# Kernel optimization log

Hardware: AMD Instinct MI355X
Metric: run time of the kernel (lower is better)

The kernel has to match this reference:

```python
import jax, jax.numpy as jnp
import numpy as np

WS = 5       # window_size
SHIFT = 2    # shift_size
NH = 3       # num_heads (hardcoded in module)
EPS = 1e-5   # LayerNorm eps (torch default)

B, H, W, C = 4, 400, 400, 48


def _window_partition(x, ws):
    b, h, w, c = x.shape
    x = x.reshape(b, h // ws, ws, w // ws, ws, c).transpose(0, 1, 3, 2, 4, 5)
    return x.reshape(-1, ws * ws, c)  # [B*nH*nW, ws*ws, C]


def _window_reverse(x, ws, h, w):
    bn = x.shape[0] // ((h // ws) * (w // ws))
    x = x.reshape(bn, h // ws, w // ws, ws, ws, -1).transpose(0, 1, 3, 2, 4, 5)
    return x.reshape(bn, h, w, -1)


def _qkv_branch(win, qkv_w, qkv_b, ln_g, ln_b):
    # Linear -> LayerNorm(last dim) -> Softmax over window-position axis (dim 1)
    y = win @ qkv_w + qkv_b                      # [B_, N, 3C]
    mu = jnp.mean(y, axis=-1, keepdims=True)
    var = jnp.mean((y - mu) ** 2, axis=-1, keepdims=True)
    y = (y - mu) * jax.lax.rsqrt(var + EPS) * ln_g + ln_b
    y = jax.nn.softmax(y, axis=1)                # nn.Softmax(1)
    b_, n, _ = y.shape
    y = y.reshape(b_, n, 3, NH, C // NH).transpose(2, 0, 3, 1, 4)  # [3, B_, h, N, d]
    return y[0], y[1], y[2]


def setup_inputs() -> dict:
    key = jax.random.key(0)
    ks = jax.random.split(key, 4)
    lr_patch = jax.random.normal(ks[0], (B, H, W, C), jnp.float32)
    ref_patch = jax.random.normal(ks[1], (B, H, W, C), jnp.float32)
    qkv_w = jax.random.normal(ks[2], (C, 3 * C), jnp.float32) * (1.0 / np.sqrt(C))
    qkv_b = jax.random.normal(ks[3], (3 * C,), jnp.float32) * 0.01
    ln_g = jnp.ones((3 * C,), jnp.float32)
    ln_b = jnp.zeros((3 * C,), jnp.float32)
    return {"lr_patch": lr_patch, "ref_patch": ref_patch, "qkv_w": qkv_w,
            "qkv_b": qkv_b, "ln_g": ln_g, "ln_b": ln_b}


def reference(lr_patch, ref_patch, qkv_w, qkv_b, ln_g, ln_b):
    # cyclic shift
    s_lr = jnp.roll(lr_patch, shift=(-SHIFT, -SHIFT), axis=(1, 2))
    s_ref = jnp.roll(ref_patch, shift=(-SHIFT, -SHIFT), axis=(1, 2))

    lr_w = _window_partition(s_lr, WS)    # [B_, N=25, C]
    ref_w = _window_partition(s_ref, WS)

    q_lr, k_lr, v_lr = _qkv_branch(lr_w, qkv_w, qkv_b, ln_g, ln_b)
    q_ref, k_ref, v_ref = _qkv_branch(ref_w, qkv_w, qkv_b, ln_g, ln_b)

    # dual cross-attention (no scaling / no second softmax, as in source)
    attn1 = jnp.einsum('bhnd,bhmd->bhnm', q_lr, k_ref)   # [B_, h, N, N]
    attn2 = jnp.einsum('bhnd,bhmd->bhnm', q_ref, k_lr)
    x = jnp.einsum('bhnm,bhmd->bhnd', attn1, v_ref)
    x = jnp.einsum('bhnm,bhmd->bhnd', attn2, x)

    b_, _, n, _ = x.shape
    x = x.transpose(0, 2, 1, 3).reshape(b_, n, C)        # [B_, N, C]
    x = x.reshape(-1, WS, WS, C)

    x = _window_reverse(x, WS, H, W)
    x = jnp.roll(x, shift=(SHIFT, SHIFT), axis=(1, 2))
    return (x, ref_patch)
```

## Files before the change

kernel.cpp:

```cpp
#include <hip/hip_runtime.h>
#include <hip/hip_bf16.h>

typedef __hip_bfloat16 hbf16;
typedef unsigned short ushort_t;
typedef __attribute__((ext_vector_type(8))) short bf16x8;
typedef __attribute__((ext_vector_type(4))) float f32x4;

#define WSZ 5
#define NWIN 25
#define CC 48
#define C3 144
#define HD 16
#define HDIM 400
#define NWH 80
#define SH 2
#define WPB 8
#define YW 152
#define WTW 56
#define PW 40

__device__ __forceinline__ ushort_t f2b(float x) {
    union { hbf16 h; ushort_t u; } c;
    c.h = __float2bfloat16(x);
    return c.u;
}
__device__ __forceinline__ float b2f_u(unsigned u) {
    union { unsigned i; float f; } c;
    c.i = u << 16;
    return c.f;
}
__device__ __forceinline__ unsigned pk2(float lo, float hi) {
    return ((unsigned)f2b(hi) << 16) | f2b(lo);
}

__global__ __launch_bounds__(256, 3) void swin_mfma(
    const float* __restrict__ lr, const float* __restrict__ ref,
    const float* __restrict__ qkv_w, const float* __restrict__ qkv_b,
    const float* __restrict__ ln_g, const float* __restrict__ ln_b,
    float* __restrict__ out)
{
    __shared__ __align__(16) ushort_t s_wT[C3 * WTW];
    __shared__ __align__(16) ushort_t s_y[64 * YW];
    __shared__ __align__(16) ushort_t s_vT[3 * 16 * PW];
    __shared__ __align__(16) ushort_t s_x1T[3 * 16 * PW];
    __shared__ __align__(16) ushort_t s_P[3 * 32 * PW];
    __shared__ float s_gb[3 * C3];

    const int tid  = threadIdx.x;
    const int wave = tid >> 6;
    const int lane = tid & 63;
    const int lm   = lane & 15;
    const int g    = lane >> 4;

    for (int i = tid; i < CC * C3; i += 256) {
        int c = i / C3, j = i % C3;
        s_wT[j * WTW + c] = f2b(qkv_w[i]);
    }
    for (int i = tid; i < C3; i += 256) {
        s_gb[i]           = qkv_b[i];
        s_gb[C3 + i]      = ln_g[i];
        s_gb[2 * C3 + i]  = ln_b[i];
    }
    for (int i = tid; i < 3 * 16 * PW; i += 256) { s_vT[i] = 0; s_x1T[i] = 0; }
    for (int i = tid; i < 3 * 32 * PW; i += 256) { s_P[i] = 0; }
    __syncthreads();

    const bf16x8 z8 = {0, 0, 0, 0, 0, 0, 0, 0};
    const f32x4  z4 = {0.f, 0.f, 0.f, 0.f};

    for (int it = 0; it < WPB; ++it) {
        const int wid = blockIdx.x * WPB + it;
        const int b   = wid / (NWH * NWH);
        const int rr  = wid % (NWH * NWH);
        const int bh  = rr / NWH;
        const int bw  = rr % NWH;

        const int pr = 16 * wave + lm;
        const bool vrow = (pr < 25) || (pr >= 32 && pr < 57);
        bf16x8 xa = z8, xb = z8;
        int n_row = (pr < 25) ? pr : pr - 32;
        {
            int wi = n_row / WSZ, wj = n_row % WSZ;
            int hh = bh * WSZ + wi + SH; if (hh >= HDIM) hh -= HDIM;
            int ww = bw * WSZ + wj + SH; if (ww >= HDIM) ww -= HDIM;
            const float* src = (pr < 32) ? lr : ref;
            const float* prow = src + ((size_t)(b * HDIM + hh) * HDIM + ww) * CC;
            if (vrow) {
                const float4* p4 = reinterpret_cast<const float4*>(prow);
                float4 u = p4[2 * g], v = p4[2 * g + 1];
                xa[0]=f2b(u.x); xa[1]=f2b(u.y); xa[2]=f2b(u.z); xa[3]=f2b(u.w);
                xa[4]=f2b(v.x); xa[5]=f2b(v.y); xa[6]=f2b(v.z); xa[7]=f2b(v.w);
                if (g < 2) {
                    float4 u2 = p4[8 + 2 * g], v2 = p4[9 + 2 * g];
                    xb[0]=f2b(u2.x); xb[1]=f2b(u2.y); xb[2]=f2b(u2.z); xb[3]=f2b(u2.w);
                    xb[4]=f2b(v2.x); xb[5]=f2b(v2.y); xb[6]=f2b(v2.z); xb[7]=f2b(v2.w);
                }
            }
        }

        f32x4 acc[9];
        const int ko2 = 32 + 8 * (g & 1);
        #pragma unroll
        for (int t = 0; t < 9; ++t) {
            const int col = 16 * t + lm;
            float bias = s_gb[col];
            f32x4 a = {bias, bias, bias, bias};
            bf16x8 w1 = *reinterpret_cast<const bf16x8*>(&s_wT[col * WTW + 8 * g]);
            a = __builtin_amdgcn_mfma_f32_16x16x32_bf16(xa, w1, a, 0, 0, 0);
            bf16x8 w2 = *reinterpret_cast<const bf16x8*>(&s_wT[col * WTW + ko2]);
            a = __builtin_amdgcn_mfma_f32_16x16x32_bf16(xb, w2, a, 0, 0, 0);
            acc[t] = a;
        }

        float mu[4], rs[4];
        #pragma unroll
        for (int r2 = 0; r2 < 4; ++r2) {
            float s = 0.f, sq = 0.f;
            #pragma unroll
            for (int t = 0; t < 9; ++t) { float v = acc[t][r2]; s += v; sq += v * v; }
            #pragma unroll
            for (int off = 8; off >= 1; off >>= 1) {
                s  += __shfl_xor(s, off);
                sq += __shfl_xor(sq, off);
            }
            float m = s * (1.f / 144.f);
            mu[r2] = m;
            rs[r2] = rsqrtf(sq * (1.f / 144.f) - m * m + 1e-5f);
        }

        const int prb = 16 * wave + 4 * g;
        #pragma unroll
        for (int t = 0; t < 9; ++t) {
            const int col = 16 * t + lm;
            const float gg = s_gb[C3 + col], bb = s_gb[2 * C3 + col];
            #pragma unroll
            for (int r2 = 0; r2 < 4; ++r2) {
                const int prow2 = prb + r2;
                const bool ok = (prow2 < 25) || (prow2 >= 32 && prow2 < 57);
                float yv = (acc[t][r2] - mu[r2]) * rs[r2] * gg + bb;
                ushort_t hv = ok ? f2b(yv) : (ushort_t)0;
                s_y[prow2 * YW + col] = hv;
            }
        }
        __syncthreads();

        #pragma unroll
        for (int ii = 0; ii < 2; ++ii) {
            const int item = wave * 72 + ii * 64 + lane;
            if (ii == 0 || lane < 8) {
                const int br  = item / C3;
                const int col = item % C3;
                const int base = br ? 32 : 0;
                float v[25];
                float mx = -1e30f;
                #pragma unroll
                for (int j = 0; j < 25; ++j) {
                    v[j] = b2f_u((unsigned)s_y[(base + j) * YW + col]);
                    mx = fmaxf(mx, v[j]);
                }
                float sum = 0.f;
                #pragma unroll
                for (int j = 0; j < 25; ++j) { v[j] = __expf(v[j] - mx); sum += v[j]; }
                float inv = 1.f / sum;
                #pragma unroll
                for (int j = 0; j < 25; ++j)
                    s_y[(base + j) * YW + col] = f2b(v[j] * inv);
            }
        }
        __syncthreads();

        for (int i = tid; i < 25 * CC; i += 256) {
            int m = i / CC, c = i % CC;
            int h2 = c >> 4, dv = c & 15;
            s_vT[h2 * (16 * PW) + dv * PW + m] = s_y[(32 + m) * YW + 96 + c];
        }
        __syncthreads();

        if (wave < 3) {
            const int h = wave;
            const int ko = 8 * (g & 1);
            f32x4 p1[2][2];
            bf16x8 ka0, ka1, qb0, qb1;
            {
                bf16x8 t0 = *reinterpret_cast<const bf16x8*>(&s_y[(32 + lm) * YW + CC + 16 * h + ko]);
                bf16x8 t1 = *reinterpret_cast<const bf16x8*>(&s_y[(48 + lm) * YW + CC + 16 * h + ko]);
                ka0 = (g < 2) ? t0 : z8;  ka1 = (g < 2) ? t1 : z8;
                bf16x8 t2 = *reinterpret_cast<const bf16x8*>(&s_y[lm * YW + 16 * h + ko]);
                bf16x8 t3 = *reinterpret_cast<const bf16x8*>(&s_y[(16 + lm) * YW + 16 * h + ko]);
                qb0 = (g < 2) ? t2 : z8;  qb1 = (g < 2) ? t3 : z8;
            }
            p1[0][0] = __builtin_amdgcn_mfma_f32_16x16x32_bf16(ka0, qb0, z4, 0, 0, 0);
            p1[0][1] = __builtin_amdgcn_mfma_f32_16x16x32_bf16(ka0, qb1, z4, 0, 0, 0);
            p1[1][0] = __builtin_amdgcn_mfma_f32_16x16x32_bf16(ka1, qb0, z4, 0, 0, 0);
            p1[1][1] = __builtin_amdgcn_mfma_f32_16x16x32_bf16(ka1, qb1, z4, 0, 0, 0);
            #pragma unroll
            for (int mt = 0; mt < 2; ++mt)
                #pragma unroll
                for (int nt = 0; nt < 2; ++nt) {
                    uint2 wv;
                    wv.x = pk2(p1[mt][nt][0], p1[mt][nt][1]);
                    wv.y = pk2(p1[mt][nt][2], p1[mt][nt][3]);
                    *reinterpret_cast<uint2*>(&s_P[h * (32 * PW) + (16 * nt + lm) * PW + 16 * mt + 4 * g]) = wv;
                }
            f32x4 x1a[2];
            {
                bf16x8 va = *reinterpret_cast<const bf16x8*>(&s_vT[h * (16 * PW) + lm * PW + 8 * g]);
                bf16x8 pb0 = *reinterpret_cast<const bf16x8*>(&s_P[h * (32 * PW) + lm * PW + 8 * g]);
                bf16x8 pb1 = *reinterpret_cast<const bf16x8*>(&s_P[h * (32 * PW) + (16 + lm) * PW + 8 * g]);
                x1a[0] = __builtin_amdgcn_mfma_f32_16x16x32_bf16(va, pb0, z4, 0, 0, 0);
                x1a[1] = __builtin_amdgcn_mfma_f32_16x16x32_bf16(va, pb1, z4, 0, 0, 0);
            }
            #pragma unroll
            for (int nt = 0; nt < 2; ++nt)
                #pragma unroll
                for (int r2 = 0; r2 < 4; ++r2)
                    s_x1T[h * (16 * PW) + (4 * g + r2) * PW + 16 * nt + lm] = f2b(x1a[nt][r2]);
            f32x4 p2[2][2];
            {
                bf16x8 t0 = *reinterpret_cast<const bf16x8*>(&s_y[lm * YW + CC + 16 * h + ko]);
                bf16x8 t1 = *reinterpret_cast<const bf16x8*>(&s_y[(16 + lm) * YW + CC + 16 * h + ko]);
                ka0 = (g < 2) ? t0 : z8;  ka1 = (g < 2) ? t1 : z8;
                bf16x8 t2 = *reinterpret_cast<const bf16x8*>(&s_y[(32 + lm) * YW + 16 * h + ko]);
                bf16x8 t3 = *reinterpret_cast<const bf16x8*>(&s_y[(48 + lm) * YW + 16 * h + ko]);
                qb0 = (g < 2) ? t2 : z8;  qb1 = (g < 2) ? t3 : z8;
            }
            p2[0][0] = __builtin_amdgcn_mfma_f32_16x16x32_bf16(ka0, qb0, z4, 0, 0, 0);
            p2[0][1] = __builtin_amdgcn_mfma_f32_16x16x32_bf16(ka0, qb1, z4, 0, 0, 0);
            p2[1][0] = __builtin_amdgcn_mfma_f32_16x16x32_bf16(ka1, qb0, z4, 0, 0, 0);
            p2[1][1] = __builtin_amdgcn_mfma_f32_16x16x32_bf16(ka1, qb1, z4, 0, 0, 0);
            #pragma unroll
            for (int mt = 0; mt < 2; ++mt)
                #pragma unroll
                for (int nt = 0; nt < 2; ++nt) {
                    uint2 wv;
                    wv.x = pk2(p2[mt][nt][0], p2[mt][nt][1]);
                    wv.y = pk2(p2[mt][nt][2], p2[mt][nt][3]);
                    *reinterpret_cast<uint2*>(&s_P[h * (32 * PW) + (16 * nt + lm) * PW + 16 * mt + 4 * g]) = wv;
                }
            {
                bf16x8 xv = *reinterpret_cast<const bf16x8*>(&s_x1T[h * (16 * PW) + lm * PW + 8 * g]);
                #pragma unroll
                for (int nt = 0; nt < 2; ++nt) {
                    bf16x8 pb = *reinterpret_cast<const bf16x8*>(&s_P[h * (32 * PW) + (16 * nt + lm) * PW + 8 * g]);
                    f32x4 x2a = __builtin_amdgcn_mfma_f32_16x16x32_bf16(xv, pb, z4, 0, 0, 0);
                    const int n = 16 * nt + lm;
                    if (n < 25) {
                        int wi = n / WSZ, wj = n % WSZ;
                        int oh = bh * WSZ + wi + SH; if (oh >= HDIM) oh -= HDIM;
                        int ow = bw * WSZ + wj + SH; if (ow >= HDIM) ow -= HDIM;
                        float4 o = make_float4(x2a[0], x2a[1], x2a[2], x2a[3]);
                        *reinterpret_cast<float4*>(
                            &out[((size_t)((b * HDIM + oh) * HDIM + ow)) * CC + 16 * h + 4 * g]) = o;
                    }
                }
            }
        }
        __syncthreads();
    }
}

__global__ void copy_ref_kernel(const float4* __restrict__ src, float4* __restrict__ dst,
                                long long n4) {
    long long i = (long long)blockIdx.x * blockDim.x + threadIdx.x;
    const long long stride = (long long)gridDim.x * blockDim.x;
    for (; i < n4; i += stride) dst[i] = src[i];
}

extern "C" void kernel_launch(void* const* d_in, const int* in_sizes, int n_in,
                              void* d_out, int out_size, void* d_ws, size_t ws_size,
                              hipStream_t stream) {
    const float* lr    = (const float*)d_in[0];
    const float* ref   = (const float*)d_in[1];
    const float* qkv_w = (const float*)d_in[2];
    const float* qkv_b = (const float*)d_in[3];
    const float* ln_g  = (const float*)d_in[4];
    const float* ln_b  = (const float*)d_in[5];
    float* out = (float*)d_out;

    const int n_blocks = 4 * NWH * NWH / WPB;
    swin_mfma<<<n_blocks, 256, 0, stream>>>(lr, ref, qkv_w, qkv_b, ln_g, ln_b, out);

    const size_t elems0 = (size_t)out_size / 2;
    const long long n4 = (long long)(elems0 / 4);
    copy_ref_kernel<<<2048, 256, 0, stream>>>(
        (const float4*)ref, (float4*)(out + elems0), n4);
}
```

Before: 329.7 us.

## Fuse ref passthrough copy into the main kernel and split QKV work across branch/column waves

```diff
diff --git a/kernel.cpp b/kernel.cpp
--- a/kernel.cpp
+++ b/kernel.cpp
@@ -2,15 +2,13 @@
 #include <hip/hip_bf16.h>
 
 typedef __hip_bfloat16 hbf16;
-typedef unsigned short ushort_t;
+typedef unsigned short u16t;
 typedef __attribute__((ext_vector_type(8))) short bf16x8;
 typedef __attribute__((ext_vector_type(4))) float f32x4;
 
 #define WSZ 5
-#define NWIN 25
 #define CC 48
 #define C3 144
-#define HD 16
 #define HDIM 400
 #define NWH 80
 #define SH 2
@@ -19,251 +17,239 @@
 #define WTW 56
 #define PW 40
 
-__device__ __forceinline__ ushort_t f2b(float x) {
-    union { hbf16 h; ushort_t u; } c;
+__device__ __forceinline__ u16t f2b(float x) {
+    union { hbf16 h; u16t u; } c;
     c.h = __float2bfloat16(x);
     return c.u;
 }
-__device__ __forceinline__ float b2f_u(unsigned u) {
-    union { unsigned i; float f; } c;
-    c.i = u << 16;
-    return c.f;
-}
 __device__ __forceinline__ unsigned pk2(float lo, float hi) {
     return ((unsigned)f2b(hi) << 16) | f2b(lo);
 }
 
-__global__ __launch_bounds__(256, 3) void swin_mfma(
+__global__ __launch_bounds__(256, 3) void swin_mfma2(
     const float* __restrict__ lr, const float* __restrict__ ref,
     const float* __restrict__ qkv_w, const float* __restrict__ qkv_b,
     const float* __restrict__ ln_g, const float* __restrict__ ln_b,
-    float* __restrict__ out)
+    float* __restrict__ out, float* __restrict__ out1)
 {
-    __shared__ __align__(16) ushort_t s_wT[C3 * WTW];
-    __shared__ __align__(16) ushort_t s_y[64 * YW];
-    __shared__ __align__(16) ushort_t s_vT[3 * 16 * PW];
-    __shared__ __align__(16) ushort_t s_x1T[3 * 16 * PW];
-    __shared__ __align__(16) ushort_t s_P[3 * 32 * PW];
-    __shared__ float s_gb[3 * C3];
-
-    const int tid  = threadIdx.x;
-    const int wave = tid >> 6;
-    const int lane = tid & 63;
-    const int lm   = lane & 15;
-    const int g    = lane >> 4;
+    __shared__ __align__(16) u16t s_wT[C3 * WTW];
+    __shared__ __align__(16) u16t s_y[64 * YW];
+    __shared__ __align__(16) u16t s_P[3 * 32 * PW];
+    __shared__ __align__(16) u16t s_x1T[3 * 16 * PW];
+    __shared__ __align__(16) float s_gb[3 * C3];
+    __shared__ __align__(16) float s_ln[4][16][4];
+
+    const int tid = threadIdx.x;
+    const int wave = tid >> 6, lane = tid & 63;
+    const int lm = lane & 15, g = lane >> 4;
+    const int br = wave >> 1, jh = wave & 1;
+    const int T0 = jh ? 4 : 0;
 
     for (int i = tid; i < CC * C3; i += 256) {
         int c = i / C3, j = i % C3;
         s_wT[j * WTW + c] = f2b(qkv_w[i]);
     }
     for (int i = tid; i < C3; i += 256) {
-        s_gb[i]           = qkv_b[i];
-        s_gb[C3 + i]      = ln_g[i];
-        s_gb[2 * C3 + i]  = ln_b[i];
+        s_gb[i] = qkv_b[i];
+        s_gb[C3 + i] = ln_g[i];
+        s_gb[2 * C3 + i] = ln_b[i];
     }
-    for (int i = tid; i < 3 * 16 * PW; i += 256) { s_vT[i] = 0; s_x1T[i] = 0; }
-    for (int i = tid; i < 3 * 32 * PW; i += 256) { s_P[i] = 0; }
     __syncthreads();
 
     const bf16x8 z8 = {0, 0, 0, 0, 0, 0, 0, 0};
     const f32x4  z4 = {0.f, 0.f, 0.f, 0.f};
+    const float* xsrc = br ? ref : lr;
 
     for (int it = 0; it < WPB; ++it) {
         const int wid = blockIdx.x * WPB + it;
-        const int b   = wid / (NWH * NWH);
-        const int rr  = wid % (NWH * NWH);
-        const int bh  = rr / NWH;
-        const int bw  = rr % NWH;
-
-        const int pr = 16 * wave + lm;
-        const bool vrow = (pr < 25) || (pr >= 32 && pr < 57);
-        bf16x8 xa = z8, xb = z8;
-        int n_row = (pr < 25) ? pr : pr - 32;
-        {
-            int wi = n_row / WSZ, wj = n_row % WSZ;
+        const int bb = wid / (NWH * NWH);
+        const int rr = wid % (NWH * NWH);
+        const int bh = rr / NWH, bw = rr % NWH;
+
+        bf16x8 xa[2], xb[2];
+        #pragma unroll
+        for (int s2 = 0; s2 < 2; ++s2) {
+            int row = 16 * s2 + lm;
+            int wi = row / WSZ, wj = row % WSZ;
             int hh = bh * WSZ + wi + SH; if (hh >= HDIM) hh -= HDIM;
             int ww = bw * WSZ + wj + SH; if (ww >= HDIM) ww -= HDIM;
-            const float* src = (pr < 32) ? lr : ref;
-            const float* prow = src + ((size_t)(b * HDIM + hh) * HDIM + ww) * CC;
-            if (vrow) {
-                const float4* p4 = reinterpret_cast<const float4*>(prow);
-                float4 u = p4[2 * g], v = p4[2 * g + 1];
-                xa[0]=f2b(u.x); xa[1]=f2b(u.y); xa[2]=f2b(u.z); xa[3]=f2b(u.w);
-                xa[4]=f2b(v.x); xa[5]=f2b(v.y); xa[6]=f2b(v.z); xa[7]=f2b(v.w);
-                if (g < 2) {
-                    float4 u2 = p4[8 + 2 * g], v2 = p4[9 + 2 * g];
-                    xb[0]=f2b(u2.x); xb[1]=f2b(u2.y); xb[2]=f2b(u2.z); xb[3]=f2b(u2.w);
-                    xb[4]=f2b(v2.x); xb[5]=f2b(v2.y); xb[6]=f2b(v2.z); xb[7]=f2b(v2.w);
+            const float4* p4 = reinterpret_cast<const float4*>(
+                xsrc + ((size_t)(bb * HDIM + hh) * HDIM + ww) * CC);
+            float4 u = p4[2 * g], v = p4[2 * g + 1];
+            bf16x8 t;
+            t[0] = f2b(u.x); t[1] = f2b(u.y); t[2] = f2b(u.z); t[3] = f2b(u.w);
+            t[4] = f2b(v.x); t[5] = f2b(v.y); t[6] = f2b(v.z); t[7] = f2b(v.w);
+            xa[s2] = t;
+            float4 u2, v2;
+            if (g < 2) {
+                u2 = p4[8 + 2 * g]; v2 = p4[9 + 2 * g];
+                bf16x8 t2;
+                t2[0] = f2b(u2.x); t2[1] = f2b(u2.y); t2[2] = f2b(u2.z); t2[3] = f2b(u2.w);
+                t2[4] = f2b(v2.x); t2[5] = f2b(v2.y); t2[6] = f2b(v2.z); t2[7] = f2b(v2.w);
+                xb[s2] = t2;
+            } else xb[s2] = z8;
+            if (wave == 3 && row < 25) {
+                float4* o1 = reinterpret_cast<float4*>(
+                    out1 + ((size_t)(bb * HDIM + hh) * HDIM + ww) * CC);
+                o1[2 * g] = u; o1[2 * g + 1] = v;
+                if (g < 2) { o1[8 + 2 * g] = u2; o1[9 + 2 * g] = v2; }
+            }
+        }
+
+        f32x4 acc[5][2];
+        #pragma unroll
+        for (int tt = 0; tt < 5; ++tt) {
+            int t = T0 + tt;
+            bf16x8 w1 = *reinterpret_cast<const bf16x8*>(&s_wT[(16 * t + lm) * WTW + 8 * g]);
+            bf16x8 w2 = *reinterpret_cast<const bf16x8*>(&s_wT[(16 * t + lm) * WTW + 32 + 8 * (g & 1)]);
+            f32x4 bv = *reinterpret_cast<const f32x4*>(&s_gb[16 * t + 4 * g]);
+            #pragma unroll
+            for (int s2 = 0; s2 < 2; ++s2) {
+                f32x4 a = bv;
+                a = __builtin_amdgcn_mfma_f32_16x16x32_bf16(w1, xa[s2], a, 0, 0, 0);
+                a = __builtin_amdgcn_mfma_f32_16x16x32_bf16(w2, xb[s2], a, 0, 0, 0);
+                acc[tt][s2] = a;
+            }
+        }
+
+        float s0 = 0.f, q0 = 0.f, s1 = 0.f, q1 = 0.f;
+        #pragma unroll
+        for (int tt = 0; tt < 5; ++tt) {
+            if (jh == 0 || tt > 0) {
+                #pragma unroll
+                for (int r2 = 0; r2 < 4; ++r2) {
+                    float va = acc[tt][0][r2]; s0 += va; q0 += va * va;
+                    float vb = acc[tt][1][r2]; s1 += vb; q1 += vb * vb;
                 }
             }
         }
-
-        f32x4 acc[9];
-        const int ko2 = 32 + 8 * (g & 1);
-        #pragma unroll
-        for (int t = 0; t < 9; ++t) {
-            const int col = 16 * t + lm;
-            float bias = s_gb[col];
-            f32x4 a = {bias, bias, bias, bias};
-            bf16x8 w1 = *reinterpret_cast<const bf16x8*>(&s_wT[col * WTW + 8 * g]);
-            a = __builtin_amdgcn_mfma_f32_16x16x32_bf16(xa, w1, a, 0, 0, 0);
-            bf16x8 w2 = *reinterpret_cast<const bf16x8*>(&s_wT[col * WTW + ko2]);
-            a = __builtin_amdgcn_mfma_f32_16x16x32_bf16(xb, w2, a, 0, 0, 0);
-            acc[t] = a;
-        }
-
-        float mu[4], rs[4];
-        #pragma unroll
-        for (int r2 = 0; r2 < 4; ++r2) {
-            float s = 0.f, sq = 0.f;
-            #pragma unroll
-            for (int t = 0; t < 9; ++t) { float v = acc[t][r2]; s += v; sq += v * v; }
-            #pragma unroll
-            for (int off = 8; off >= 1; off >>= 1) {
-                s  += __shfl_xor(s, off);
-                sq += __shfl_xor(sq, off);
-            }
-            float m = s * (1.f / 144.f);
-            mu[r2] = m;
-            rs[r2] = rsqrtf(sq * (1.f / 144.f) - m * m + 1e-5f);
-        }
-
-        const int prb = 16 * wave + 4 * g;
-        #pragma unroll
-        for (int t = 0; t < 9; ++t) {
-            const int col = 16 * t + lm;
-            const float gg = s_gb[C3 + col], bb = s_gb[2 * C3 + col];
+        s0 += __shfl_xor(s0, 16); s0 += __shfl_xor(s0, 32);
+        q0 += __shfl_xor(q0, 16); q0 += __shfl_xor(q0, 32);
+        s1 += __shfl_xor(s1, 16); s1 += __shfl_xor(s1, 32);
+        q1 += __shfl_xor(q1, 16); q1 += __shfl_xor(q1, 32);
+        if (lane < 16) {
+            float4 w4 = make_float4(s0, q0, s1, q1);
+            *reinterpret_cast<float4*>(&s_ln[wave][lm][0]) = w4;
+        }
+        __syncthreads();
+        {
+            float4 p = *reinterpret_cast<const float4*>(&s_ln[wave ^ 1][lm][0]);
+            float S0 = s0 + p.x, Q0 = q0 + p.y, S1 = s1 + p.z, Q1 = q1 + p.w;
+            float mu0 = S0 * (1.f / 144.f);
+            float rs0 = rsqrtf(Q0 * (1.f / 144.f) - mu0 * mu0 + 1e-5f);
+            float mu1 = S1 * (1.f / 144.f);
+            float rs1 = rsqrtf(Q1 * (1.f / 144.f) - mu1 * mu1 + 1e-5f);
+            #pragma unroll
+            for (int tt = 0; tt < 5; ++tt) {
+                int t = T0 + tt;
+                f32x4 gv = *reinterpret_cast<const f32x4*>(&s_gb[C3 + 16 * t + 4 * g]);
+                f32x4 bv2 = *reinterpret_cast<const f32x4*>(&s_gb[2 * C3 + 16 * t + 4 * g]);
+                #pragma unroll
+                for (int r2 = 0; r2 < 4; ++r2) {
+                    acc[tt][0][r2] = (acc[tt][0][r2] - mu0) * rs0 * gv[r2] + bv2[r2];
+                    acc[tt][1][r2] = (acc[tt][1][r2] - mu1) * rs1 * gv[r2] + bv2[r2];
+                }
+            }
+        }
+
+        #pragma unroll
+        for (int tt = 0; tt < 5; ++tt) {
+            int t = T0 + tt;
+            float pa[4], pb[4];
             #pragma unroll
             for (int r2 = 0; r2 < 4; ++r2) {
-                const int prow2 = prb + r2;
-                const bool ok = (prow2 < 25) || (prow2 >= 32 && prow2 < 57);
-                float yv = (acc[t][r2] - mu[r2]) * rs[r2] * gg + bb;
-                ushort_t hv = ok ? f2b(yv) : (ushort_t)0;
-                s_y[prow2 * YW + col] = hv;
-            }
-        }
-        __syncthreads();
-
-        #pragma unroll
-        for (int ii = 0; ii < 2; ++ii) {
-            const int item = wave * 72 + ii * 64 + lane;
-            if (ii == 0 || lane < 8) {
-                const int br  = item / C3;
-                const int col = item % C3;
-                const int base = br ? 32 : 0;
-                float v[25];
-                float mx = -1e30f;
-                #pragma unroll
-                for (int j = 0; j < 25; ++j) {
-                    v[j] = b2f_u((unsigned)s_y[(base + j) * YW + col]);
-                    mx = fmaxf(mx, v[j]);
-                }
-                float sum = 0.f;
-                #pragma unroll
-                for (int j = 0; j < 25; ++j) { v[j] = __expf(v[j] - mx); sum += v[j]; }
-                float inv = 1.f / sum;
-                #pragma unroll
-                for (int j = 0; j < 25; ++j)
-                    s_y[(base + j) * YW + col] = f2b(v[j] * inv);
-            }
-        }
-        __syncthreads();
-
-        for (int i = tid; i < 25 * CC; i += 256) {
-            int m = i / CC, c = i % CC;
-            int h2 = c >> 4, dv = c & 15;
-            s_vT[h2 * (16 * PW) + dv * PW + m] = s_y[(32 + m) * YW + 96 + c];
+                float va = acc[tt][0][r2];
+                float vb = (lm < 9) ? acc[tt][1][r2] : -1e30f;
+                float m = fmaxf(va, vb);
+                m = fmaxf(m, __shfl_xor(m, 1)); m = fmaxf(m, __shfl_xor(m, 2));
+                m = fmaxf(m, __shfl_xor(m, 4)); m = fmaxf(m, __shfl_xor(m, 8));
+                float ea = __expf(va - m), eb = __expf(vb - m);
+                float ss = ea + eb;
+                ss += __shfl_xor(ss, 1); ss += __shfl_xor(ss, 2);
+                ss += __shfl_xor(ss, 4); ss += __shfl_xor(ss, 8);
+                float inv = __builtin_amdgcn_rcpf(ss);
+                pa[r2] = ea * inv; pb[r2] = eb * inv;
+            }
+            int colw = 16 * t + 4 * g;
+            uint2 wv;
+            wv.x = pk2(pa[0], pa[1]); wv.y = pk2(pa[2], pa[3]);
+            *reinterpret_cast<uint2*>(&s_y[(32 * br + lm) * YW + colw]) = wv;
+            wv.x = pk2(pb[0], pb[1]); wv.y = pk2(pb[2], pb[3]);
+            *reinterpret_cast<uint2*>(&s_y[(32 * br + 16 + lm) * YW + colw]) = wv;
         }
         __syncthreads();
 
         if (wave < 3) {
             const int h = wave;
             const int ko = 8 * (g & 1);
-            f32x4 p1[2][2];
-            bf16x8 ka0, ka1, qb0, qb1;
-            {
-                bf16x8 t0 = *reinterpret_cast<const bf16x8*>(&s_y[(32 + lm) * YW + CC + 16 * h + ko]);
-                bf16x8 t1 = *reinterpret_cast<const bf16x8*>(&s_y[(48 + lm) * YW + CC + 16 * h + ko]);
-                ka0 = (g < 2) ? t0 : z8;  ka1 = (g < 2) ? t1 : z8;
-                bf16x8 t2 = *reinterpret_cast<const bf16x8*>(&s_y[lm * YW + 16 * h + ko]);
-                bf16x8 t3 = *reinterpret_cast<const bf16x8*>(&s_y[(16 + lm) * YW + 16 * h + ko]);
-                qb0 = (g < 2) ? t2 : z8;  qb1 = (g < 2) ? t3 : z8;
-            }
-            p1[0][0] = __builtin_amdgcn_mfma_f32_16x16x32_bf16(ka0, qb0, z4, 0, 0, 0);
-            p1[0][1] = __builtin_amdgcn_mfma_f32_16x16x32_bf16(ka0, qb1, z4, 0, 0, 0);
-            p1[1][0] = __builtin_amdgcn_mfma_f32_16x16x32_bf16(ka1, qb0, z4, 0, 0, 0);
-            p1[1][1] = __builtin_amdgcn_mfma_f32_16x16x32_bf16(ka1, qb1, z4, 0, 0, 0);
-            #pragma unroll
-            for (int mt = 0; mt < 2; ++mt)
-                #pragma unroll
-                for (int nt = 0; nt < 2; ++nt) {
-                    uint2 wv;
-                    wv.x = pk2(p1[mt][nt][0], p1[mt][nt][1]);
-                    wv.y = pk2(p1[mt][nt][2], p1[mt][nt][3]);
-                    *reinterpret_cast<uint2*>(&s_P[h * (32 * PW) + (16 * nt + lm) * PW + 16 * mt + 4 * g]) = wv;
+            const bool gok = (g < 2);
+            u16t* Ph = &s_P[h * 32 * PW];
+            u16t* Xh = &s_x1T[h * 16 * PW];
+            bf16x8 ka0 = gok ? *reinterpret_cast<const bf16x8*>(&s_y[(32 + lm) * YW + CC + 16 * h + ko]) : z8;
+            bf16x8 ka1 = gok ? *reinterpret_cast<const bf16x8*>(&s_y[(48 + lm) * YW + CC + 16 * h + ko]) : z8;
+            bf16x8 qb0 = *reinterpret_cast<const bf16x8*>(&s_y[lm * YW + 16 * h + ko]);
+            bf16x8 qb1 = *reinterpret_cast<const bf16x8*>(&s_y[(16 + lm) * YW + 16 * h + ko]);
+            f32x4 p00 = __builtin_amdgcn_mfma_f32_16x16x32_bf16(ka0, qb0, z4, 0, 0, 0);
+            f32x4 p01 = __builtin_amdgcn_mfma_f32_16x16x32_bf16(ka0, qb1, z4, 0, 0, 0);
+            f32x4 p10 = __builtin_amdgcn_mfma_f32_16x16x32_bf16(ka1, qb0, z4, 0, 0, 0);
+            f32x4 p11 = __builtin_amdgcn_mfma_f32_16x16x32_bf16(ka1, qb1, z4, 0, 0, 0);
+            uint2 wv;
+            wv.x = pk2(p00[0], p00[1]); wv.y = pk2(p00[2], p00[3]);
+            *reinterpret_cast<uint2*>(&Ph[lm * PW + 4 * g]) = wv;
+            wv.x = pk2(p01[0], p01[1]); wv.y = pk2(p01[2], p01[3]);
+            *reinterpret_cast<uint2*>(&Ph[(16 + lm) * PW + 4 * g]) = wv;
+            wv.x = pk2(p10[0], p10[1]); wv.y = pk2(p10[2], p10[3]);
+            *reinterpret_cast<uint2*>(&Ph[lm * PW + 16 + 4 * g]) = wv;
+            wv.x = pk2(p11[0], p11[1]); wv.y = pk2(p11[2], p11[3]);
+            *reinterpret_cast<uint2*>(&Ph[(16 + lm) * PW + 16 + 4 * g]) = wv;
+            bf16x8 vfr;
+            #pragma unroll
+            for (int j = 0; j < 8; ++j)
+                vfr[j] = (short)s_y[(32 + 8 * g + j) * YW + 96 + 16 * h + lm];
+            bf16x8 a0 = *reinterpret_cast<const bf16x8*>(&Ph[lm * PW + 8 * g]);
+            bf16x8 a1 = *reinterpret_cast<const bf16x8*>(&Ph[(16 + lm) * PW + 8 * g]);
+            f32x4 x10 = __builtin_amdgcn_mfma_f32_16x16x32_bf16(a0, vfr, z4, 0, 0, 0);
+            f32x4 x11 = __builtin_amdgcn_mfma_f32_16x16x32_bf16(a1, vfr, z4, 0, 0, 0);
+            wv.x = pk2(x10[0], x10[1]); wv.y = pk2(x10[2], x10[3]);
+            *reinterpret_cast<uint2*>(&Xh[lm * PW + 4 * g]) = wv;
+            wv.x = pk2(x11[0], x11[1]); wv.y = pk2(x11[2], x11[3]);
+            *reinterpret_cast<uint2*>(&Xh[lm * PW + 16 + 4 * g]) = wv;
+            bf16x8 kb0 = gok ? *reinterpret_cast<const bf16x8*>(&s_y[lm * YW + CC + 16 * h + ko]) : z8;
+            bf16x8 kb1 = gok ? *reinterpret_cast<const bf16x8*>(&s_y[(16 + lm) * YW + CC + 16 * h + ko]) : z8;
+            bf16x8 qc0 = *reinterpret_cast<const bf16x8*>(&s_y[(32 + lm) * YW + 16 * h + ko]);
+            bf16x8 qc1 = *reinterpret_cast<const bf16x8*>(&s_y[(48 + lm) * YW + 16 * h + ko]);
+            p00 = __builtin_amdgcn_mfma_f32_16x16x32_bf16(kb0, qc0, z4, 0, 0, 0);
+            p01 = __builtin_amdgcn_mfma_f32_16x16x32_bf16(kb0, qc1, z4, 0, 0, 0);
+            p10 = __builtin_amdgcn_mfma_f32_16x16x32_bf16(kb1, qc0, z4, 0, 0, 0);
+            p11 = __builtin_amdgcn_mfma_f32_16x16x32_bf16(kb1, qc1, z4, 0, 0, 0);
+            wv.x = pk2(p00[0], p00[1]); wv.y = pk2(p00[2], p00[3]);
+            *reinterpret_cast<uint2*>(&Ph[lm * PW + 4 * g]) = wv;
+            wv.x = pk2(p01[0], p01[1]); wv.y = pk2(p01[2], p01[3]);
+            *reinterpret_cast<uint2*>(&Ph[(16 + lm) * PW + 4 * g]) = wv;
+            wv.x = pk2(p10[0], p10[1]); wv.y = pk2(p10[2], p10[3]);
+            *reinterpret_cast<uint2*>(&Ph[lm * PW + 16 + 4 * g]) = wv;
+            wv.x = pk2(p11[0], p11[1]); wv.y = pk2(p11[2], p11[3]);
+            *reinterpret_cast<uint2*>(&Ph[(16 + lm) * PW + 16 + 4 * g]) = wv;
+            bf16x8 xv = *reinterpret_cast<const bf16x8*>(&Xh[lm * PW + 8 * g]);
+            bf16x8 pb0 = *reinterpret_cast<const bf16x8*>(&Ph[lm * PW + 8 * g]);
+            bf16x8 pb1 = *reinterpret_cast<const bf16x8*>(&Ph[(16 + lm) * PW + 8 * g]);
+            f32x4 o0 = __builtin_amdgcn_mfma_f32_16x16x32_bf16(xv, pb0, z4, 0, 0, 0);
+            f32x4 o1v = __builtin_amdgcn_mfma_f32_16x16x32_bf16(xv, pb1, z4, 0, 0, 0);
+            #pragma unroll
+            for (int nt = 0; nt < 2; ++nt) {
+                int n2 = 16 * nt + lm;
+                if (n2 < 25) {
+                    f32x4 ov = nt ? o1v : o0;
+                    int wi2 = n2 / WSZ, wj2 = n2 % WSZ;
+                    int oh = bh * WSZ + wi2 + SH; if (oh >= HDIM) oh -= HDIM;
+                    int ow = bw * WSZ + wj2 + SH; if (ow >= HDIM) ow -= HDIM;
+                    float4 o = make_float4(ov[0], ov[1], ov[2], ov[3]);
+                    *reinterpret_cast<float4*>(
+                        &out[((size_t)(bb * HDIM + oh) * HDIM + ow) * CC + 16 * h + 4 * g]) = o;
                 }
-            f32x4 x1a[2];
-            {
-                bf16x8 va = *reinterpret_cast<const bf16x8*>(&s_vT[h * (16 * PW) + lm * PW + 8 * g]);
-                bf16x8 pb0 = *reinterpret_cast<const bf16x8*>(&s_P[h * (32 * PW) + lm * PW + 8 * g]);
-                bf16x8 pb1 = *reinterpret_cast<const bf16x8*>(&s_P[h * (32 * PW) + (16 + lm) * PW + 8 * g]);
-                x1a[0] = __builtin_amdgcn_mfma_f32_16x16x32_bf16(va, pb0, z4, 0, 0, 0);
-                x1a[1] = __builtin_amdgcn_mfma_f32_16x16x32_bf16(va, pb1, z4, 0, 0, 0);
-            }
-            #pragma unroll
-            for (int nt = 0; nt < 2; ++nt)
-                #pragma unroll
-                for (int r2 = 0; r2 < 4; ++r2)
-                    s_x1T[h * (16 * PW) + (4 * g + r2) * PW + 16 * nt + lm] = f2b(x1a[nt][r2]);
-            f32x4 p2[2][2];
-            {
-                bf16x8 t0 = *reinterpret_cast<const bf16x8*>(&s_y[lm * YW + CC + 16 * h + ko]);
-                bf16x8 t1 = *reinterpret_cast<const bf16x8*>(&s_y[(16 + lm) * YW + CC + 16 * h + ko]);
-                ka0 = (g < 2) ? t0 : z8;  ka1 = (g < 2) ? t1 : z8;
-                bf16x8 t2 = *reinterpret_cast<const bf16x8*>(&s_y[(32 + lm) * YW + 16 * h + ko]);
-                bf16x8 t3 = *reinterpret_cast<const bf16x8*>(&s_y[(48 + lm) * YW + 16 * h + ko]);
-                qb0 = (g < 2) ? t2 : z8;  qb1 = (g < 2) ? t3 : z8;
-            }
-            p2[0][0] = __builtin_amdgcn_mfma_f32_16x16x32_bf16(ka0, qb0, z4, 0, 0, 0);
-            p2[0][1] = __builtin_amdgcn_mfma_f32_16x16x32_bf16(ka0, qb1, z4, 0, 0, 0);
-            p2[1][0] = __builtin_amdgcn_mfma_f32_16x16x32_bf16(ka1, qb0, z4, 0, 0, 0);
-            p2[1][1] = __builtin_amdgcn_mfma_f32_16x16x32_bf16(ka1, qb1, z4, 0, 0, 0);
-            #pragma unroll
-            for (int mt = 0; mt < 2; ++mt)
-                #pragma unroll
-                for (int nt = 0; nt < 2; ++nt) {
-                    uint2 wv;
-                    wv.x = pk2(p2[mt][nt][0], p2[mt][nt][1]);
-                    wv.y = pk2(p2[mt][nt][2], p2[mt][nt][3]);
-                    *reinterpret_cast<uint2*>(&s_P[h * (32 * PW) + (16 * nt + lm) * PW + 16 * mt + 4 * g]) = wv;
-                }
-            {
-                bf16x8 xv = *reinterpret_cast<const bf16x8*>(&s_x1T[h * (16 * PW) + lm * PW + 8 * g]);
-                #pragma unroll
-                for (int nt = 0; nt < 2; ++nt) {
-                    bf16x8 pb = *reinterpret_cast<const bf16x8*>(&s_P[h * (32 * PW) + (16 * nt + lm) * PW + 8 * g]);
-                    f32x4 x2a = __builtin_amdgcn_mfma_f32_16x16x32_bf16(xv, pb, z4, 0, 0, 0);
-                    const int n = 16 * nt + lm;
-                    if (n < 25) {
-                        int wi = n / WSZ, wj = n % WSZ;
-                        int oh = bh * WSZ + wi + SH; if (oh >= HDIM) oh -= HDIM;
-                        int ow = bw * WSZ + wj + SH; if (ow >= HDIM) ow -= HDIM;
-                        float4 o = make_float4(x2a[0], x2a[1], x2a[2], x2a[3]);
-                        *reinterpret_cast<float4*>(
-                            &out[((size_t)((b * HDIM + oh) * HDIM + ow)) * CC + 16 * h + 4 * g]) = o;
-                    }
-                }
-            }
-        }
-        __syncthreads();
+            }
+        }
     }
-}
-
-__global__ void copy_ref_kernel(const float4* __restrict__ src, float4* __restrict__ dst,
-                                long long n4) {
-    long long i = (long long)blockIdx.x * blockDim.x + threadIdx.x;
-    const long long stride = (long long)gridDim.x * blockDim.x;
-    for (; i < n4; i += stride) dst[i] = src[i];
 }
 
 extern "C" void kernel_launch(void* const* d_in, const int* in_sizes, int n_in,
@@ -276,12 +262,8 @@
     const float* ln_g  = (const float*)d_in[4];
     const float* ln_b  = (const float*)d_in[5];
     float* out = (float*)d_out;
+    float* out1 = out + (size_t)out_size / 2;
 
     const int n_blocks = 4 * NWH * NWH / WPB;
-    swin_mfma<<<n_blocks, 256, 0, stream>>>(lr, ref, qkv_w, qkv_b, ln_g, ln_b, out);
-
-    const size_t elems0 = (size_t)out_size / 2;
-    const long long n4 = (long long)(elems0 / 4);
-    copy_ref_kernel<<<2048, 256, 0, stream>>>(
-        (const float4*)ref, (float4*)(out + elems0), n4);
-}
+    swin_mfma2<<<n_blocks, 256, 0, stream>>>(lr, ref, qkv_w, qkv_b, ln_g, ln_b, out, out1);
+}
```

After: 333.6 us. No clear change (+1.2%).
